# Kernel optimization log

Measured on AMD Instinct MI355X. Metric: run time of the kernel, lower is better.

## Reference

```python
import jax, jax.numpy as jnp
import numpy as np

B, L, IN_DIM, H, DK, DV = 4, 512, 256, 8, 32, 32
TEMP = DK ** 0.5  # temperature = d_k ** 0.5
LN_EPS = 1e-6


def setup_inputs() -> dict:
    key = jax.random.key(0)
    ks = jax.random.split(key, 5)
    s = 0.05
    return {
        "x": jax.random.normal(ks[0], (B, L, IN_DIM), jnp.float32),
        "w_q": jax.random.normal(ks[1], (IN_DIM, H * DK), jnp.float32) * s,
        "w_k": jax.random.normal(ks[2], (IN_DIM, H * DK), jnp.float32) * s,
        "w_v": jax.random.normal(ks[3], (IN_DIM, H * DV), jnp.float32) * s,
        "w_fc": jax.random.normal(ks[4], (H * DV, IN_DIM), jnp.float32) * s,
        "ln_gamma": jnp.ones((IN_DIM,), jnp.float32),
        "ln_beta": jnp.zeros((IN_DIM,), jnp.float32),
    }


def reference(x, w_q, w_k, w_v, w_fc, ln_gamma, ln_beta):
    # LayerNorm (biased variance, eps inside sqrt, as in torch.nn.LayerNorm)
    mu = jnp.mean(x, axis=-1, keepdims=True)
    var = jnp.var(x, axis=-1, keepdims=True)
    xn = (x - mu) / jnp.sqrt(var + LN_EPS) * ln_gamma + ln_beta
    residual = xn

    # Projections; torch layout after transpose(1,3) is [B, d, H, L]; per-head slice is [B, d, L].
    # We use [B, H, d, L] which yields identical per-head tensors (vectorized over heads).
    q = (xn @ w_q).reshape(B, L, H, DK).transpose(0, 2, 3, 1) / TEMP  # [B,H,DK,L]
    k = (xn @ w_k).reshape(B, L, H, DK).transpose(0, 2, 3, 1)          # [B,H,DK,L]
    v = (xn @ w_v).reshape(B, L, H, DV).transpose(0, 2, 3, 1)          # [B,H,DV,L]

    # L1 distance scores (note the source's index convention):
    # attn[b,h,i,j] = mean_d |q[b,h,d,j] - k[b,h,d,i]|   -> [B,H,L,L]
    attn = jnp.mean(jnp.abs(q[:, :, :, None, :] - k[:, :, :, :, None]), axis=2)
    attn = jax.nn.softmax(attn, axis=-1)

    # out[b,h,d,i] = sum_j v[b,h,d,j] * attn[b,h,i,j]   (torch: bmm(v, attn^T))
    out = jnp.einsum('bhdj,bhij->bhdi', v, attn)  # [B,H,DV,L]
    out = out.reshape(B, H * DV, L).transpose(0, 2, 1)  # head-major concat -> [B,L,H*DV]
    out = out @ w_fc + residual  # use_gamma=False path; dropout is identity at eval

    # extract_attn_map (no_grad in source)
    am = jax.lax.stop_gradient(attn)
    am = jnp.mean(am, axis=1)          # mean over heads -> [B,L,L]
    am = jnp.sum(am, axis=1)           # sum over key axis -> [B,L]
    mn = jnp.min(am, axis=1, keepdims=True)
    mx = jnp.max(am, axis=1, keepdims=True)
    am = (am - mn) / (mx - mn)
    return out, am
```

## Files before the change

kernel.cpp:

```cpp
#include <hip/hip_runtime.h>
#include <hip/hip_fp16.h>
#include <math.h>

#define BATCH 4
#define SEQ   512
#define IND   256
#define NH    8
#define DKV   32
#define BH    32
#define NTOK  2048

typedef __attribute__((ext_vector_type(8))) short short8v;
typedef __attribute__((ext_vector_type(4))) float floatx4;

__device__ __forceinline__ unsigned f2bf1(float f) {
    unsigned u = __builtin_bit_cast(unsigned, f);
    return (u + 0x7fffu + ((u >> 16) & 1u)) >> 16;
}
__device__ __forceinline__ unsigned f2bf2(float lo, float hi) {
    return f2bf1(lo) | (f2bf1(hi) << 16);
}
__device__ __forceinline__ __half2 habs2_(__half2 x) {
    unsigned u = __builtin_bit_cast(unsigned, x) & 0x7fff7fffu;
    return __builtin_bit_cast(__half2, u);
}

__global__ __launch_bounds__(256) void lnproj_kernel(
        const float* __restrict__ x,
        const float* __restrict__ gamma, const float* __restrict__ beta,
        const float* __restrict__ wq, const float* __restrict__ wk,
        const float* __restrict__ wv,
        float* __restrict__ xn, float* __restrict__ am,
        __half* __restrict__ Q, __half* __restrict__ K,
        unsigned short* __restrict__ Vt) {
    __shared__ __align__(16) unsigned short As[64][264];
    __shared__ __align__(16) unsigned short Bs[2][64][40];
    const int t = threadIdx.x;
    const int m0 = blockIdx.x * 64;
    const int y = blockIdx.y;
    const int which = y >> 2;
    const int n0 = (y & 3) * 64;
    const float* W = (which == 0) ? wq : (which == 1) ? wk : wv;

    {
        const int r = t >> 2, q = t & 3;
        const float* xr = x + (m0 + r) * IND + q * 64;
        float4 xv[16];
        float s = 0.0f, s2 = 0.0f;
        #pragma unroll
        for (int i = 0; i < 16; i++) {
            xv[i] = *(const float4*)&xr[i * 4];
            s  += xv[i].x + xv[i].y + xv[i].z + xv[i].w;
            s2 += xv[i].x * xv[i].x + xv[i].y * xv[i].y
                + xv[i].z * xv[i].z + xv[i].w * xv[i].w;
        }
        s  += __shfl_xor(s, 1, 64);  s  += __shfl_xor(s, 2, 64);
        s2 += __shfl_xor(s2, 1, 64); s2 += __shfl_xor(s2, 2, 64);
        float mu = s * (1.0f / IND);
        float var = s2 * (1.0f / IND) - mu * mu;
        float rinv = rsqrtf(var + 1e-6f);
        const bool dox = (y == 0);
        if (dox && t < 64) am[m0 + t] = 0.0f;
        #pragma unroll
        for (int i = 0; i < 8; i++) {
            float4 a = xv[2 * i], bv = xv[2 * i + 1];
            float4 g0 = *(const float4*)&gamma[q * 64 + i * 8];
            float4 g1 = *(const float4*)&gamma[q * 64 + i * 8 + 4];
            float4 b0 = *(const float4*)&beta[q * 64 + i * 8];
            float4 b1 = *(const float4*)&beta[q * 64 + i * 8 + 4];
            float4 n0v, n1v;
            n0v.x = (a.x - mu) * rinv * g0.x + b0.x;
            n0v.y = (a.y - mu) * rinv * g0.y + b0.y;
            n0v.z = (a.z - mu) * rinv * g0.z + b0.z;
            n0v.w = (a.w - mu) * rinv * g0.w + b0.w;
            n1v.x = (bv.x - mu) * rinv * g1.x + b1.x;
            n1v.y = (bv.y - mu) * rinv * g1.y + b1.y;
            n1v.z = (bv.z - mu) * rinv * g1.z + b1.z;
            n1v.w = (bv.w - mu) * rinv * g1.w + b1.w;
            if (dox) {
                *(float4*)&xn[(m0 + r) * IND + q * 64 + i * 8] = n0v;
                *(float4*)&xn[(m0 + r) * IND + q * 64 + i * 8 + 4] = n1v;
            }
            uint4 pk;
            pk.x = f2bf2(n0v.x, n0v.y); pk.y = f2bf2(n0v.z, n0v.w);
            pk.z = f2bf2(n1v.x, n1v.y); pk.w = f2bf2(n1v.z, n1v.w);
            *(uint4*)&As[r][q * 64 + i * 8] = pk;
        }
    }

    const int w = t >> 6, l = t & 63;
    const int wm = (w >> 1) * 32, wn = (w & 1) * 32;
    const int fr = l & 15, fg = l >> 4;
    floatx4 acc[2][2];
    #pragma unroll
    for (int i = 0; i < 2; i++)
        #pragma unroll
        for (int j = 0; j < 2; j++) acc[i][j] = (floatx4)(0.0f);

    const int kl = t >> 4, nq = t & 15;
    auto stageB = [&](int kt, int buf) {
        float4 b0 = *(const float4*)&W[(kt * 32 + kl) * IND + n0 + nq * 4];
        float4 b1 = *(const float4*)&W[(kt * 32 + 16 + kl) * IND + n0 + nq * 4];
        Bs[buf][nq * 4 + 0][kl] = (unsigned short)f2bf1(b0.x);
        Bs[buf][nq * 4 + 1][kl] = (unsigned short)f2bf1(b0.y);
        Bs[buf][nq * 4 + 2][kl] = (unsigned short)f2bf1(b0.z);
        Bs[buf][nq * 4 + 3][kl] = (unsigned short)f2bf1(b0.w);
        Bs[buf][nq * 4 + 0][kl + 16] = (unsigned short)f2bf1(b1.x);
        Bs[buf][nq * 4 + 1][kl + 16] = (unsigned short)f2bf1(b1.y);
        Bs[buf][nq * 4 + 2][kl + 16] = (unsigned short)f2bf1(b1.z);
        Bs[buf][nq * 4 + 3][kl + 16] = (unsigned short)f2bf1(b1.w);
    };
    stageB(0, 0);
    __syncthreads();
    #pragma unroll
    for (int kt = 0; kt < 8; kt++) {
        if (kt < 7) stageB(kt + 1, (kt + 1) & 1);
        const int buf = kt & 1;
        short8v a0 = *(const short8v*)&As[wm + fr][kt * 32 + fg * 8];
        short8v a1 = *(const short8v*)&As[wm + 16 + fr][kt * 32 + fg * 8];
        short8v b0 = *(const short8v*)&Bs[buf][wn + fr][fg * 8];
        short8v b1 = *(const short8v*)&Bs[buf][wn + 16 + fr][fg * 8];
        acc[0][0] = __builtin_amdgcn_mfma_f32_16x16x32_bf16(a0, b0, acc[0][0], 0, 0, 0);
        acc[0][1] = __builtin_amdgcn_mfma_f32_16x16x32_bf16(a0, b1, acc[0][1], 0, 0, 0);
        acc[1][0] = __builtin_amdgcn_mfma_f32_16x16x32_bf16(a1, b0, acc[1][0], 0, 0, 0);
        acc[1][1] = __builtin_amdgcn_mfma_f32_16x16x32_bf16(a1, b1, acc[1][1], 0, 0, 0);
        __syncthreads();
    }

    const float scale = (which == 0) ? 0.17677669529663687f : 1.0f;
    #pragma unroll
    for (int mi = 0; mi < 2; mi++)
        #pragma unroll
        for (int ni = 0; ni < 2; ni++)
            #pragma unroll
            for (int reg = 0; reg < 4; reg++) {
                int row = m0 + wm + mi * 16 + fg * 4 + reg;
                int col = n0 + wn + ni * 16 + fr;
                int b = row >> 9, ll = row & 511;
                int h = col >> 5, d = col & 31;
                if (which == 2) {
                    Vt[(((b << 3) + h) * DKV + d) * SEQ + ll] =
                        (unsigned short)f2bf1(acc[mi][ni][reg]);
                } else {
                    __half* O = (which == 0) ? Q : K;
                    O[(((b << 3) + h) * SEQ + ll) * DKV + d] =
                        __float2half_rn(acc[mi][ni][reg] * scale);
                }
            }
}

__global__ __launch_bounds__(256) void attn_kernel(
        const __half* __restrict__ Qh, const __half* __restrict__ Kh,
        const unsigned short* __restrict__ Vt,
        float* __restrict__ attn_out, float* __restrict__ am) {
    __shared__ __align__(16) unsigned char ldsraw[2 * 128 * 40 * 2];
    __half (*Th)[128][40] = (__half (*)[128][40])ldsraw;
    unsigned short (*Pl)[520] = (unsigned short (*)[520])ldsraw;
    const int t = threadIdx.x;
    const int l = t & 63;
    const int g = t >> 5, jl = t & 31;
    const int li = l & 15, jc = l >> 4;
    const int w = t >> 6;
    const int gy = blockIdx.y;
    const int i0 = blockIdx.x * 16;
    const int b = gy >> 3, h = gy & 7;
    const __half* Qb = Qh + gy * SEQ * DKV;
    const __half* Kb = Kh + gy * SEQ * DKV;
    const unsigned short* Vb = Vt + gy * DKV * SEQ;
    const int r0 = t >> 2, ch = t & 3;

    __half2 ka[16], kb[16];
    {
        const float4* pa = (const float4*)(Kb + (i0 + g) * DKV);
        const float4* pb = (const float4*)(Kb + (i0 + g + 8) * DKV);
        #pragma unroll
        for (int c = 0; c < 4; c++) {
            float4 va = pa[c], vb = pb[c];
            const __half2* ha = (const __half2*)&va;
            const __half2* hb = (const __half2*)&vb;
            #pragma unroll
            for (int k = 0; k < 4; k++) { ka[c*4+k] = ha[k]; kb[c*4+k] = hb[k]; }
        }
    }

    float vals_a[16], vals_b[16];
    float4 pre0, pre1;

    pre0 = *(const float4*)(Qb + r0 * DKV + ch * 8);
    pre1 = *(const float4*)(Qb + (r0 + 64) * DKV + ch * 8);
    *(float4*)&Th[0][r0][ch * 8] = pre0;
    *(float4*)&Th[0][r0 + 64][ch * 8] = pre1;
    __syncthreads();
    #pragma unroll
    for (int tile = 0; tile < 4; tile++) {
        const int buf = tile & 1;
        if (tile < 3) {
            pre0 = *(const float4*)(Qb + ((tile+1)*128 + r0) * DKV + ch * 8);
            pre1 = *(const float4*)(Qb + ((tile+1)*128 + r0 + 64) * DKV + ch * 8);
        }
        #pragma unroll
        for (int m = 0; m < 4; m++) {
            const int j = jl + m * 32;
            __half2 z = __float2half2_rn(0.0f);
            __half2 sa0 = z, sa1 = z, sb0 = z, sb1 = z;
            #pragma unroll
            for (int c = 0; c < 4; c++) {
                float4 qv = *(const float4*)&Th[buf][j][c * 8];
                const __half2* q2 = (const __half2*)&qv;
                #pragma unroll
                for (int k = 0; k < 4; k++) {
                    __half2 da = habs2_(__hsub2(q2[k], ka[c*4+k]));
                    __half2 db = habs2_(__hsub2(q2[k], kb[c*4+k]));
                    if (k & 1) { sa1 = __hadd2(sa1, da); sb1 = __hadd2(sb1, db); }
                    else       { sa0 = __hadd2(sa0, da); sb0 = __hadd2(sb0, db); }
                }
            }
            __half2 sa = __hadd2(sa0, sa1), sb = __hadd2(sb0, sb1);
            vals_a[tile*4+m] = (__low2float(sa) + __high2float(sa)) * (1.0f/32.0f);
            vals_b[tile*4+m] = (__low2float(sb) + __high2float(sb)) * (1.0f/32.0f);
        }
        if (tile < 3) {
            *(float4*)&Th[buf ^ 1][r0][ch * 8] = pre0;
            *(float4*)&Th[buf ^ 1][r0 + 64][ch * 8] = pre1;
        }
        __syncthreads();
    }

    float mxa = vals_a[0], mxb = vals_b[0];
    #pragma unroll
    for (int m = 1; m < 16; m++) {
        mxa = fmaxf(mxa, vals_a[m]); mxb = fmaxf(mxb, vals_b[m]);
    }
    #pragma unroll
    for (int s = 1; s <= 16; s <<= 1) {
        mxa = fmaxf(mxa, __shfl_xor(mxa, s, 64));
        mxb = fmaxf(mxb, __shfl_xor(mxb, s, 64));
    }
    float sua = 0.0f, sub = 0.0f;
    #pragma unroll
    for (int m = 0; m < 16; m++) {
        vals_a[m] = __expf(vals_a[m] - mxa); sua += vals_a[m];
        vals_b[m] = __expf(vals_b[m] - mxb); sub += vals_b[m];
    }
    #pragma unroll
    for (int s = 1; s <= 16; s <<= 1) {
        sua += __shfl_xor(sua, s, 64);
        sub += __shfl_xor(sub, s, 64);
    }
    float inva = 1.0f / sua, invb = 1.0f / sub;
    #pragma unroll
    for (int m = 0; m < 16; m++) { vals_a[m] *= inva; vals_b[m] *= invb; }

    #pragma unroll
    for (int m = 0; m < 16; m++) {
        const int j = (m >> 2) * 128 + (m & 3) * 32 + jl;
        Pl[g][j]     = (unsigned short)f2bf1(vals_a[m]);
        Pl[g + 8][j] = (unsigned short)f2bf1(vals_b[m]);
    }
    __syncthreads();

    floatx4 oacc[2];
    oacc[0] = (floatx4)(0.0f); oacc[1] = (floatx4)(0.0f);
    #pragma unroll
    for (int jt = 0; jt < 16; jt++) {
        short8v pa = *(const short8v*)&Pl[li][jt * 32 + jc * 8];
        #pragma unroll
        for (int n = 0; n < 2; n++) {
            short8v bf = *(const short8v*)&Vb[(n * 16 + li) * SEQ + jt * 32 + jc * 8];
            oacc[n] = __builtin_amdgcn_mfma_f32_16x16x32_bf16(pa, bf, oacc[n], 0, 0, 0);
        }
    }
    if (jc == w) {
        #pragma unroll
        for (int n = 0; n < 2; n++)
            #pragma unroll
            for (int r = 0; r < 4; r++)
                attn_out[(b * SEQ + i0 + jc * 4 + r) * IND + h * 32 + n * 16 + li] =
                    oacc[n][r];
    }

    {
        const int jp = t * 2;
        float cs0 = 0.0f, cs1 = 0.0f;
        #pragma unroll
        for (int i = 0; i < 16; i++) {
            unsigned u = *(const unsigned*)&Pl[i][jp];
            cs0 += __builtin_bit_cast(float, u << 16);
            cs1 += __builtin_bit_cast(float, u & 0xffff0000u);
        }
        atomicAdd(&am[b * SEQ + jp],     cs0 * 0.125f);
        atomicAdd(&am[b * SEQ + jp + 1], cs1 * 0.125f);
    }
}

__global__ __launch_bounds__(256) void fcam_kernel(
        const float* __restrict__ ao, const float* __restrict__ wfc,
        const float* __restrict__ xn, const float* __restrict__ am,
        float* __restrict__ out, float* __restrict__ out_am) {
    __shared__ __align__(16) unsigned short As[64][264];
    __shared__ __align__(16) unsigned short Bs[2][64][40];
    __shared__ float lmn[4], lmx[4];
    const int t = threadIdx.x;

    if (blockIdx.x == 32) {
        int b = blockIdx.y;
        float v0 = am[b * SEQ + t];
        float v1 = am[b * SEQ + t + 256];
        float mn = fminf(v0, v1), mx = fmaxf(v0, v1);
        #pragma unroll
        for (int o = 32; o > 0; o >>= 1) {
            mn = fminf(mn, __shfl_xor(mn, o, 64));
            mx = fmaxf(mx, __shfl_xor(mx, o, 64));
        }
        int w = t >> 6;
        if ((t & 63) == 0) { lmn[w] = mn; lmx[w] = mx; }
        __syncthreads();
        mn = fminf(fminf(lmn[0], lmn[1]), fminf(lmn[2], lmn[3]));
        mx = fmaxf(fmaxf(lmx[0], lmx[1]), fmaxf(lmx[2], lmx[3]));
        float inv = 1.0f / (mx - mn);
        out_am[b * SEQ + t]       = (v0 - mn) * inv;
        out_am[b * SEQ + t + 256] = (v1 - mn) * inv;
        return;
    }

    const int m0 = blockIdx.x * 64;
    const int n0 = blockIdx.y * 64;

    {
        const int r = t >> 2, q = t & 3;
        const float* ar = ao + (m0 + r) * IND + q * 64;
        #pragma unroll
        for (int i = 0; i < 8; i++) {
            float4 a = *(const float4*)&ar[i * 8];
            float4 bv = *(const float4*)&ar[i * 8 + 4];
            uint4 pk;
            pk.x = f2bf2(a.x, a.y);  pk.y = f2bf2(a.z, a.w);
            pk.z = f2bf2(bv.x, bv.y); pk.w = f2bf2(bv.z, bv.w);
            *(uint4*)&As[r][q * 64 + i * 8] = pk;
        }
    }

    const int w = t >> 6, l = t & 63;
    const int wm = (w >> 1) * 32, wn = (w & 1) * 32;
    const int fr = l & 15, fg = l >> 4;
    floatx4 acc[2][2];
    #pragma unroll
    for (int i = 0; i < 2; i++)
        #pragma unroll
        for (int j = 0; j < 2; j++) acc[i][j] = (floatx4)(0.0f);

    const int kl = t >> 4, nq = t & 15;
    auto stageB = [&](int kt, int buf) {
        float4 b0 = *(const float4*)&wfc[(kt * 32 + kl) * IND + n0 + nq * 4];
        float4 b1 = *(const float4*)&wfc[(kt * 32 + 16 + kl) * IND + n0 + nq * 4];
        Bs[buf][nq * 4 + 0][kl] = (unsigned short)f2bf1(b0.x);
        Bs[buf][nq * 4 + 1][kl] = (unsigned short)f2bf1(b0.y);
        Bs[buf][nq * 4 + 2][kl] = (unsigned short)f2bf1(b0.z);
        Bs[buf][nq * 4 + 3][kl] = (unsigned short)f2bf1(b0.w);
        Bs[buf][nq * 4 + 0][kl + 16] = (unsigned short)f2bf1(b1.x);
        Bs[buf][nq * 4 + 1][kl + 16] = (unsigned short)f2bf1(b1.y);
        Bs[buf][nq * 4 + 2][kl + 16] = (unsigned short)f2bf1(b1.z);
        Bs[buf][nq * 4 + 3][kl + 16] = (unsigned short)f2bf1(b1.w);
    };
    stageB(0, 0);
    __syncthreads();
    #pragma unroll
    for (int kt = 0; kt < 8; kt++) {
        if (kt < 7) stageB(kt + 1, (kt + 1) & 1);
        const int buf = kt & 1;
        short8v a0 = *(const short8v*)&As[wm + fr][kt * 32 + fg * 8];
        short8v a1 = *(const short8v*)&As[wm + 16 + fr][kt * 32 + fg * 8];
        short8v b0 = *(const short8v*)&Bs[buf][wn + fr][fg * 8];
        short8v b1 = *(const short8v*)&Bs[buf][wn + 16 + fr][fg * 8];
        acc[0][0] = __builtin_amdgcn_mfma_f32_16x16x32_bf16(a0, b0, acc[0][0], 0, 0, 0);
        acc[0][1] = __builtin_amdgcn_mfma_f32_16x16x32_bf16(a0, b1, acc[0][1], 0, 0, 0);
        acc[1][0] = __builtin_amdgcn_mfma_f32_16x16x32_bf16(a1, b0, acc[1][0], 0, 0, 0);
        acc[1][1] = __builtin_amdgcn_mfma_f32_16x16x32_bf16(a1, b1, acc[1][1], 0, 0, 0);
        __syncthreads();
    }

    #pragma unroll
    for (int mi = 0; mi < 2; mi++)
        #pragma unroll
        for (int ni = 0; ni < 2; ni++)
            #pragma unroll
            for (int reg = 0; reg < 4; reg++) {
                int row = m0 + wm + mi * 16 + fg * 4 + reg;
                int col = n0 + wn + ni * 16 + fr;
                out[row * IND + col] = acc[mi][ni][reg] + xn[row * IND + col];
            }
}

extern "C" void kernel_launch(void* const* d_in, const int* in_sizes, int n_in,
                              void* d_out, int out_size, void* d_ws, size_t ws_size,
                              hipStream_t stream) {
    (void)in_sizes; (void)n_in; (void)out_size; (void)ws_size;
    const float* x     = (const float*)d_in[0];
    const float* w_q   = (const float*)d_in[1];
    const float* w_k   = (const float*)d_in[2];
    const float* w_v   = (const float*)d_in[3];
    const float* w_fc  = (const float*)d_in[4];
    const float* gamma = (const float*)d_in[5];
    const float* beta  = (const float*)d_in[6];
    float* out = (float*)d_out;

    float* ws = (float*)d_ws;
    float* xn = ws;
    float* AO = xn + NTOK * IND;
    float* AM = AO + NTOK * IND;
    __half* Qh = (__half*)(AM + NTOK);
    __half* Kh = Qh + BH * SEQ * DKV;
    unsigned short* Vb16 = (unsigned short*)(Kh + BH * SEQ * DKV);

    hipLaunchKernelGGL(lnproj_kernel, dim3(32, 12), dim3(256), 0, stream,
                       x, gamma, beta, w_q, w_k, w_v, xn, AM, Qh, Kh, Vb16);
    hipLaunchKernelGGL(attn_kernel, dim3(32, 32), dim3(256), 0, stream,
                       Qh, Kh, Vb16, AO, AM);
    hipLaunchKernelGGL(fcam_kernel, dim3(33, 4), dim3(256), 0, stream,
                       AO, w_fc, xn, AM, out, out + NTOK * IND);
}
```

Measured before the change: 79.48 us.

## Split attention into score and PV kernels with deferred softmax normalisation

Splits the fused attention kernel into two. The first computes L1 scores over half the key range per block (grid z=2), writes unnormalised exp values as bf16 to a global P buffer, and atomically accumulates row sums into R. The second reloads P, runs the PV MFMA, and divides by R at output and in the attention-map column sums. The goal is to double the number of score blocks for better occupancy. In exchange it adds a 16 MB bf16 global round trip and an extra launch, and it drops max subtraction, which is safe only because the scores are bounded L1 means.

Result: slower. 89.06 us (+12.1%).

```diff
diff --git a/kernel.cpp b/kernel.cpp
--- a/kernel.cpp
+++ b/kernel.cpp
@@ -30,7 +30,7 @@
         const float* __restrict__ gamma, const float* __restrict__ beta,
         const float* __restrict__ wq, const float* __restrict__ wk,
         const float* __restrict__ wv,
-        float* __restrict__ xn, float* __restrict__ am,
+        float* __restrict__ xn, float* __restrict__ am, float* __restrict__ R,
         __half* __restrict__ Q, __half* __restrict__ K,
         unsigned short* __restrict__ Vt) {
     __shared__ __align__(16) unsigned short As[64][264];
@@ -60,7 +60,11 @@
         float var = s2 * (1.0f / IND) - mu * mu;
         float rinv = rsqrtf(var + 1e-6f);
         const bool dox = (y == 0);
-        if (dox && t < 64) am[m0 + t] = 0.0f;
+        if (dox) {
+            if (t < 64) am[m0 + t] = 0.0f;
+            R[blockIdx.x * 512 + t] = 0.0f;
+            R[blockIdx.x * 512 + 256 + t] = 0.0f;
+        }
         #pragma unroll
         for (int i = 0; i < 8; i++) {
             float4 a = xv[2 * i], bv = xv[2 * i + 1];
@@ -149,24 +153,18 @@
             }
 }
 
-__global__ __launch_bounds__(256) void attn_kernel(
+__global__ __launch_bounds__(256) void attn_score_kernel(
         const __half* __restrict__ Qh, const __half* __restrict__ Kh,
-        const unsigned short* __restrict__ Vt,
-        float* __restrict__ attn_out, float* __restrict__ am) {
-    __shared__ __align__(16) unsigned char ldsraw[2 * 128 * 40 * 2];
-    __half (*Th)[128][40] = (__half (*)[128][40])ldsraw;
-    unsigned short (*Pl)[520] = (unsigned short (*)[520])ldsraw;
+        unsigned short* __restrict__ Pg,
+        float* __restrict__ R) {
+    __shared__ __align__(16) __half Th[2][128][40];
     const int t = threadIdx.x;
-    const int l = t & 63;
     const int g = t >> 5, jl = t & 31;
-    const int li = l & 15, jc = l >> 4;
-    const int w = t >> 6;
     const int gy = blockIdx.y;
     const int i0 = blockIdx.x * 16;
-    const int b = gy >> 3, h = gy & 7;
+    const int jz = blockIdx.z * 256;
     const __half* Qb = Qh + gy * SEQ * DKV;
     const __half* Kb = Kh + gy * SEQ * DKV;
-    const unsigned short* Vb = Vt + gy * DKV * SEQ;
     const int r0 = t >> 2, ch = t & 3;
 
     __half2 ka[16], kb[16];
@@ -183,20 +181,20 @@
         }
     }
 
-    float vals_a[16], vals_b[16];
+    float vals_a[8], vals_b[8];
     float4 pre0, pre1;
 
-    pre0 = *(const float4*)(Qb + r0 * DKV + ch * 8);
-    pre1 = *(const float4*)(Qb + (r0 + 64) * DKV + ch * 8);
+    pre0 = *(const float4*)(Qb + (jz + r0) * DKV + ch * 8);
+    pre1 = *(const float4*)(Qb + (jz + r0 + 64) * DKV + ch * 8);
     *(float4*)&Th[0][r0][ch * 8] = pre0;
     *(float4*)&Th[0][r0 + 64][ch * 8] = pre1;
     __syncthreads();
     #pragma unroll
-    for (int tile = 0; tile < 4; tile++) {
+    for (int tile = 0; tile < 2; tile++) {
         const int buf = tile & 1;
-        if (tile < 3) {
-            pre0 = *(const float4*)(Qb + ((tile+1)*128 + r0) * DKV + ch * 8);
-            pre1 = *(const float4*)(Qb + ((tile+1)*128 + r0 + 64) * DKV + ch * 8);
+        if (tile < 1) {
+            pre0 = *(const float4*)(Qb + (jz + 128 + r0) * DKV + ch * 8);
+            pre1 = *(const float4*)(Qb + (jz + 128 + r0 + 64) * DKV + ch * 8);
         }
         #pragma unroll
         for (int m = 0; m < 4; m++) {
@@ -219,44 +217,64 @@
             vals_a[tile*4+m] = (__low2float(sa) + __high2float(sa)) * (1.0f/32.0f);
             vals_b[tile*4+m] = (__low2float(sb) + __high2float(sb)) * (1.0f/32.0f);
         }
-        if (tile < 3) {
+        if (tile < 1) {
             *(float4*)&Th[buf ^ 1][r0][ch * 8] = pre0;
             *(float4*)&Th[buf ^ 1][r0 + 64][ch * 8] = pre1;
         }
         __syncthreads();
     }
 
-    float mxa = vals_a[0], mxb = vals_b[0];
-    #pragma unroll
-    for (int m = 1; m < 16; m++) {
-        mxa = fmaxf(mxa, vals_a[m]); mxb = fmaxf(mxb, vals_b[m]);
-    }
-    #pragma unroll
-    for (int s = 1; s <= 16; s <<= 1) {
-        mxa = fmaxf(mxa, __shfl_xor(mxa, s, 64));
-        mxb = fmaxf(mxb, __shfl_xor(mxb, s, 64));
-    }
     float sua = 0.0f, sub = 0.0f;
     #pragma unroll
-    for (int m = 0; m < 16; m++) {
-        vals_a[m] = __expf(vals_a[m] - mxa); sua += vals_a[m];
-        vals_b[m] = __expf(vals_b[m] - mxb); sub += vals_b[m];
+    for (int m = 0; m < 8; m++) {
+        vals_a[m] = __expf(vals_a[m]); sua += vals_a[m];
+        vals_b[m] = __expf(vals_b[m]); sub += vals_b[m];
     }
     #pragma unroll
     for (int s = 1; s <= 16; s <<= 1) {
         sua += __shfl_xor(sua, s, 64);
         sub += __shfl_xor(sub, s, 64);
     }
-    float inva = 1.0f / sua, invb = 1.0f / sub;
-    #pragma unroll
-    for (int m = 0; m < 16; m++) { vals_a[m] *= inva; vals_b[m] *= invb; }
-
-    #pragma unroll
-    for (int m = 0; m < 16; m++) {
-        const int j = (m >> 2) * 128 + (m & 3) * 32 + jl;
-        Pl[g][j]     = (unsigned short)f2bf1(vals_a[m]);
-        Pl[g + 8][j] = (unsigned short)f2bf1(vals_b[m]);
-    }
+    if (jl == 0) {
+        atomicAdd(&R[gy * SEQ + i0 + g], sua);
+        atomicAdd(&R[gy * SEQ + i0 + g + 8], sub);
+    }
+
+    unsigned short* Pa = Pg + (gy * SEQ + i0 + g) * SEQ;
+    unsigned short* Pb = Pg + (gy * SEQ + i0 + g + 8) * SEQ;
+    #pragma unroll
+    for (int m = 0; m < 8; m++) {
+        const int j = jz + (m >> 2) * 128 + (m & 3) * 32 + jl;
+        Pa[j] = (unsigned short)f2bf1(vals_a[m]);
+        Pb[j] = (unsigned short)f2bf1(vals_b[m]);
+    }
+}
+
+__global__ __launch_bounds__(256) void attn_pv_kernel(
+        const unsigned short* __restrict__ Pg, const float* __restrict__ R,
+        const unsigned short* __restrict__ Vt,
+        float* __restrict__ attn_out, float* __restrict__ am) {
+    __shared__ __align__(16) unsigned short Pl[16][520];
+    __shared__ float Rv[16];
+    const int t = threadIdx.x;
+    const int l = t & 63, w = t >> 6;
+    const int li = l & 15, jc = l >> 4;
+    const int gy = blockIdx.y;
+    const int i0 = blockIdx.x * 16;
+    const int b = gy >> 3, h = gy & 7;
+    const unsigned short* Vb = Vt + gy * DKV * SEQ;
+
+    {
+        const unsigned short* Ps = Pg + (gy * SEQ + i0) * SEQ;
+        const int row = t >> 4;
+        #pragma unroll
+        for (int k = 0; k < 4; k++) {
+            const int chunk = (t & 15) + 16 * k;
+            *(uint4*)&Pl[row][chunk * 8] =
+                *(const uint4*)&Ps[row * SEQ + chunk * 8];
+        }
+    }
+    if (t < 16) Rv[t] = 1.0f / R[gy * SEQ + i0 + t];
     __syncthreads();
 
     floatx4 oacc[2];
@@ -272,11 +290,13 @@
     }
     if (jc == w) {
         #pragma unroll
-        for (int n = 0; n < 2; n++)
+        for (int r = 0; r < 4; r++) {
+            const float rinv = Rv[jc * 4 + r];
             #pragma unroll
-            for (int r = 0; r < 4; r++)
+            for (int n = 0; n < 2; n++)
                 attn_out[(b * SEQ + i0 + jc * 4 + r) * IND + h * 32 + n * 16 + li] =
-                    oacc[n][r];
+                    oacc[n][r] * rinv;
+        }
     }
 
     {
@@ -285,8 +305,9 @@
         #pragma unroll
         for (int i = 0; i < 16; i++) {
             unsigned u = *(const unsigned*)&Pl[i][jp];
-            cs0 += __builtin_bit_cast(float, u << 16);
-            cs1 += __builtin_bit_cast(float, u & 0xffff0000u);
+            const float ri = Rv[i];
+            cs0 += __builtin_bit_cast(float, u << 16) * ri;
+            cs1 += __builtin_bit_cast(float, u & 0xffff0000u) * ri;
         }
         atomicAdd(&am[b * SEQ + jp],     cs0 * 0.125f);
         atomicAdd(&am[b * SEQ + jp + 1], cs1 * 0.125f);
@@ -408,14 +429,18 @@
     float* xn = ws;
     float* AO = xn + NTOK * IND;
     float* AM = AO + NTOK * IND;
-    __half* Qh = (__half*)(AM + NTOK);
+    float* R  = AM + NTOK;
+    __half* Qh = (__half*)(R + BH * SEQ);
     __half* Kh = Qh + BH * SEQ * DKV;
     unsigned short* Vb16 = (unsigned short*)(Kh + BH * SEQ * DKV);
+    unsigned short* Pg = Vb16 + BH * SEQ * DKV;
 
     hipLaunchKernelGGL(lnproj_kernel, dim3(32, 12), dim3(256), 0, stream,
-                       x, gamma, beta, w_q, w_k, w_v, xn, AM, Qh, Kh, Vb16);
-    hipLaunchKernelGGL(attn_kernel, dim3(32, 32), dim3(256), 0, stream,
-                       Qh, Kh, Vb16, AO, AM);
+                       x, gamma, beta, w_q, w_k, w_v, xn, AM, R, Qh, Kh, Vb16);
+    hipLaunchKernelGGL(attn_score_kernel, dim3(32, 32, 2), dim3(256), 0, stream,
+                       Qh, Kh, Pg, R);
+    hipLaunchKernelGGL(attn_pv_kernel, dim3(32, 32), dim3(256), 0, stream,
+                       Pg, R, Vb16, AO, AM);
     hipLaunchKernelGGL(fcam_kernel, dim3(33, 4), dim3(256), 0, stream,
                        AO, w_fc, xn, AM, out, out + NTOK * IND);
 }
```
